# Optimization experiments

Measured on AMD Instinct MI355X. Metric: run time of the kernel, lower is better.

The kernel has to match this reference:

```python
import jax, jax.numpy as jnp
import numpy as np

N_DRUG, N_CELL, N_GENE = 2048, 2048, 4096
N = N_DRUG + N_CELL + N_GENE
E = 262144
H1, H2, H3, HEADS = 256, 64, 64, 4
N_PAIRS = 10000
EPS = 1e-5


def _gatv2(x, src, dst, Wl, bl, Wr, br, att, bias, heads, out_ch):
    # PyG GATv2Conv: e_ij = att . leaky_relu(Wl x_j + Wr x_i), softmax over incoming edges of i,
    # out_i = sum_j alpha_ij * (Wl x_j), heads concatenated, plus output bias.
    n = x.shape[0]
    xl = (x @ Wl + bl).reshape(n, heads, out_ch)   # source transform
    xr = (x @ Wr + br).reshape(n, heads, out_ch)   # target transform
    e = jax.nn.leaky_relu(xl[src] + xr[dst], 0.2)  # [E, H, C]
    logits = jnp.einsum('ehc,hc->eh', e, att)      # [E, H]
    m = jax.ops.segment_max(logits, dst, num_segments=n)
    ex = jnp.exp(logits - m[dst])
    denom = jax.ops.segment_sum(ex, dst, num_segments=n)
    alpha = ex / denom[dst]                        # [E, H]
    out = jax.ops.segment_sum(xl[src] * alpha[:, :, None], dst, num_segments=n)
    return out.reshape(n, heads * out_ch) + bias, alpha


def _graph_norm(x, gamma, beta, mscale):
    # PyG GraphNorm over a single graph: out = (x - a*mean) / sqrt(var + eps) * gamma + beta
    mu = x.mean(0)
    sub = x - mu * mscale
    var = (sub * sub).mean(0)
    return sub / jnp.sqrt(var + EPS) * gamma + beta


def setup_inputs() -> dict:
    key = jax.random.key(0)
    ks = jax.random.split(key, 24)
    f = jnp.float32
    nrm = lambda k, shape, sc: jax.random.normal(k, shape, f) * sc
    drug = jax.random.normal(ks[0], (N_DRUG, N_DRUG), f)
    cell = jax.random.normal(ks[1], (N_CELL, N_CELL), f)
    gene = jax.random.normal(ks[2], (N_GENE, N_GENE), f)
    # random edges guaranteed to have no self loops (PyG would remove then re-add them)
    src = jax.random.randint(ks[3], (E,), 0, N)
    off = jax.random.randint(ks[4], (E,), 1, N)
    edges = jnp.stack([src, (src + off) % N]).astype(jnp.int32)
    idx_drug = jax.random.randint(ks[5], (N_PAIRS,), 0, N_DRUG)
    idx_cell = N_DRUG + jax.random.randint(ks[6], (N_PAIRS,), 0, N_CELL)
    HC2, HC3 = HEADS * H2, HEADS * H3
    return {
        'drug': drug, 'cell': cell, 'gene': gene,
        'edges': edges, 'idx_drug': idx_drug, 'idx_cell': idx_cell,
        'W_drug': nrm(ks[7], (N_DRUG, H1), 1 / np.sqrt(N_DRUG)), 'b_drug': jnp.zeros((H1,), f),
        'W_cell': nrm(ks[8], (N_CELL, H1), 1 / np.sqrt(N_CELL)), 'b_cell': jnp.zeros((H1,), f),
        'W_gene': nrm(ks[9], (N_GENE, H1), 1 / np.sqrt(N_GENE)), 'b_gene': jnp.zeros((H1,), f),
        'gat1_Wl': nrm(ks[10], (H1, HC2), 1 / np.sqrt(H1)), 'gat1_bl': jnp.zeros((HC2,), f),
        'gat1_Wr': nrm(ks[11], (H1, HC2), 1 / np.sqrt(H1)), 'gat1_br': jnp.zeros((HC2,), f),
        'gat1_att': nrm(ks[12], (HEADS, H2), 1 / np.sqrt(H2)), 'gat1_bias': jnp.zeros((HC2,), f),
        'gat2_Wl': nrm(ks[13], (HC2, HC3), 1 / np.sqrt(HC2)), 'gat2_bl': jnp.zeros((HC3,), f),
        'gat2_Wr': nrm(ks[14], (HC2, HC3), 1 / np.sqrt(HC2)), 'gat2_br': jnp.zeros((HC3,), f),
        'gat2_att': nrm(ks[15], (HEADS, H3), 1 / np.sqrt(H3)), 'gat2_bias': jnp.zeros((HC3,), f),
        'gn1_gamma': jnp.ones((HC2,), f), 'gn1_beta': jnp.zeros((HC2,), f), 'gn1_scale': jnp.ones((HC2,), f),
        'gn2_gamma': jnp.ones((HC3,), f), 'gn2_beta': jnp.zeros((HC3,), f), 'gn2_scale': jnp.ones((HC3,), f),
        'lin1_W': nrm(ks[16], (2 * HC3, 1), 1 / np.sqrt(2 * HC3)), 'lin1_b': jnp.zeros((1,), f),
    }


def reference(drug, cell, gene, edges, idx_drug, idx_cell,
              W_drug, b_drug, W_cell, b_cell, W_gene, b_gene,
              gat1_Wl, gat1_bl, gat1_Wr, gat1_br, gat1_att, gat1_bias,
              gat2_Wl, gat2_bl, gat2_Wr, gat2_br, gat2_att, gat2_bias,
              gn1_gamma, gn1_beta, gn1_scale, gn2_gamma, gn2_beta, gn2_scale,
              lin1_W, lin1_b):
    x = jnp.concatenate([drug @ W_drug + b_drug,
                         cell @ W_cell + b_cell,
                         gene @ W_gene + b_gene], axis=0)  # [N, H1]
    loops = jnp.arange(N, dtype=edges.dtype)
    src = jnp.concatenate([edges[0], loops])  # GATv2Conv adds self loops
    dst = jnp.concatenate([edges[1], loops])
    x, a1 = _gatv2(x, src, dst, gat1_Wl, gat1_bl, gat1_Wr, gat1_br, gat1_att, gat1_bias, HEADS, H2)
    x = jax.nn.relu(_graph_norm(x, gn1_gamma, gn1_beta, gn1_scale))  # dropout = identity (eval)
    x, a2 = _gatv2(x, src, dst, gat2_Wl, gat2_bl, gat2_Wr, gat2_br, gat2_att, gat2_bias, HEADS, H3)
    x = jax.nn.relu(_graph_norm(x, gn2_gamma, gn2_beta, gn2_scale))
    pair = jnp.concatenate([x[idx_drug], x[idx_cell]], axis=1)  # [P, 2*H*H3]
    pred = jax.nn.sigmoid(pair @ lin1_W + lin1_b)
    # get_attention_mat: dense [N,N], every edge position set to the (detached) scalar mean of
    # attention weights; the two layer matrices share edge positions so they simply add.
    val = jax.lax.stop_gradient(a1.mean() + a2.mean())
    attn = jnp.zeros((N, N), x.dtype).at[src, dst].set(val)
    return pred, attn
```

## Files before the change

### kernel.cpp

```cpp
#include <hip/hip_runtime.h>

#define NNODES 8192
#define NEDGE  262144
#define EETOT  270336
#define NPAIRS 10000

typedef __attribute__((ext_vector_type(8))) short s16x8;
typedef __attribute__((ext_vector_type(8))) unsigned short u16x8;
typedef __attribute__((ext_vector_type(4))) float f32x4;

__device__ __forceinline__ float lrelu(float v) { return v > 0.f ? v : 0.2f * v; }

__device__ __forceinline__ void split2(float a, unsigned short& h, unsigned short& l) {
  unsigned u = __float_as_uint(a);
  h = (unsigned short)(u >> 16);
  float hf = __uint_as_float(u & 0xffff0000u);
  float r = a - hf;
  unsigned v = __float_as_uint(r);
  v += 0x7fffu + ((v >> 16) & 1u);
  l = (unsigned short)(v >> 16);
}

__device__ __forceinline__ unsigned short f2bf(float f) {
  unsigned u = __float_as_uint(f);
  u += 0x7fffu + ((u >> 16) & 1u);
  return (unsigned short)(u >> 16);
}
__device__ __forceinline__ float bf2f(unsigned short u) {
  return __uint_as_float((unsigned)u << 16);
}

__device__ __forceinline__ void wsplit_body(const float* __restrict__ W,
    unsigned short* __restrict__ Th, int K, int blk) {
  int col = threadIdx.x;
  int kb = blk * 8;
  u16x8 vh;
#pragma unroll
  for (int i = 0; i < 8; ++i)
    vh[i] = f2bf(W[(size_t)(kb + i) * 256 + col]);
  *(u16x8*)(Th + (size_t)col * K + kb) = vh;
}

__global__ __launch_bounds__(256) void k_wsplit_all(
    const float* __restrict__ Wd, const float* __restrict__ Wc, const float* __restrict__ Wg,
    const float* __restrict__ W1l, const float* __restrict__ W1r,
    const float* __restrict__ W2l, const float* __restrict__ W2r,
    unsigned short* __restrict__ tdh, unsigned short* __restrict__ tch,
    unsigned short* __restrict__ tgh,
    unsigned short* __restrict__ tl1h, unsigned short* __restrict__ tr1h,
    unsigned short* __restrict__ tl2h, unsigned short* __restrict__ tr2h,
    int* __restrict__ counts_d, int* __restrict__ counts_s, float* __restrict__ stats) {
  int b = blockIdx.x;
  if      (b < 256)  wsplit_body(Wd,  tdh, 2048, b);
  else if (b < 512)  wsplit_body(Wc,  tch, 2048, b - 256);
  else if (b < 1024) wsplit_body(Wg,  tgh, 4096, b - 512);
  else if (b < 1056) { wsplit_body(W1l, tl1h, 256, b - 1024);
                       counts_d[(b - 1024) * 256 + threadIdx.x] = 0; }
  else if (b < 1088) { wsplit_body(W1r, tr1h, 256, b - 1056);
                       counts_s[(b - 1056) * 256 + threadIdx.x] = 0; }
  else if (b < 1120) { wsplit_body(W2l, tl2h, 256, b - 1088);
                       if (b < 1092) stats[(b - 1088) * 256 + threadIdx.x] = 0.f; }
  else               wsplit_body(W2r, tr2h, 256, b - 1120);
}

struct Tile128 {
  unsigned short Ah[128][40], Al[128][40], Bh[128][40];
};
struct TileN {
  Tile128 t;
  float nsc[256], nsh[256];
};

template<bool BIAS, bool OUTBF, bool NORM>
__device__ __forceinline__ void gemm_tile128(Tile128& s,
    const float* __restrict__ A, int lda,
    const unsigned short* __restrict__ Th, int ldb, int nsteps,
    const float* __restrict__ bias, float* __restrict__ C,
    unsigned short* __restrict__ Cb,
    const float* __restrict__ nsc, const float* __restrict__ nsh) {
  const int tid = threadIdx.x;
  const int wave = tid >> 6, lane = tid & 63;
  const int g = lane >> 4, r = lane & 15;
  const int wr = (wave >> 1) * 64, wc = (wave & 1) * 64;

  const int ar = tid >> 1, ak = (tid & 1) * 16;
  const float* Arow = A + (size_t)ar * lda + ak;
  const int bc = tid & 127, bk = (tid >> 7) * 16;
  const unsigned short* Bhs = Th + (size_t)bc * ldb + bk;

  f32x4 acc[4][4];
#pragma unroll
  for (int m = 0; m < 4; ++m)
#pragma unroll
    for (int n = 0; n < 4; ++n)
#pragma unroll
      for (int j = 0; j < 4; ++j) acc[m][n][j] = 0.f;

  float4 pa0 = *(const float4*)(Arow);
  float4 pa1 = *(const float4*)(Arow + 4);
  float4 pa2 = *(const float4*)(Arow + 8);
  float4 pa3 = *(const float4*)(Arow + 12);
  u16x8 ph0 = *(const u16x8*)(Bhs);
  u16x8 ph1 = *(const u16x8*)(Bhs + 8);

  for (int t = 0; t < nsteps; ++t) {
    {
      float av[16] = {pa0.x, pa0.y, pa0.z, pa0.w, pa1.x, pa1.y, pa1.z, pa1.w,
                      pa2.x, pa2.y, pa2.z, pa2.w, pa3.x, pa3.y, pa3.z, pa3.w};
      u16x8 vh0, vh1, vl0, vl1;
#pragma unroll
      for (int i = 0; i < 16; ++i) {
        float v = av[i];
        if constexpr (NORM) {
          int ch = t * 32 + ak + i;
          v = fmaxf(v * nsc[ch] + nsh[ch], 0.f);
        }
        unsigned short hh, ll;
        split2(v, hh, ll);
        if (i < 8) { vh0[i] = hh; vl0[i] = ll; }
        else       { vh1[i - 8] = hh; vl1[i - 8] = ll; }
      }
      *(u16x8*)&s.Ah[ar][ak]     = vh0;
      *(u16x8*)&s.Ah[ar][ak + 8] = vh1;
      *(u16x8*)&s.Al[ar][ak]     = vl0;
      *(u16x8*)&s.Al[ar][ak + 8] = vl1;
      *(u16x8*)&s.Bh[bc][bk]     = ph0;
      *(u16x8*)&s.Bh[bc][bk + 8] = ph1;
    }
    __syncthreads();
    if (t + 1 < nsteps) {
      const float* An = Arow + (size_t)(t + 1) * 32;
      pa0 = *(const float4*)(An);
      pa1 = *(const float4*)(An + 4);
      pa2 = *(const float4*)(An + 8);
      pa3 = *(const float4*)(An + 12);
      const unsigned short* Bhn = Bhs + (size_t)(t + 1) * 32;
      ph0 = *(const u16x8*)(Bhn);
      ph1 = *(const u16x8*)(Bhn + 8);
    }
    s16x8 fah[4], fal[4], fbh[4];
#pragma unroll
    for (int m = 0; m < 4; ++m) {
      fah[m] = *(const s16x8*)&s.Ah[wr + m * 16 + r][g * 8];
      fal[m] = *(const s16x8*)&s.Al[wr + m * 16 + r][g * 8];
    }
#pragma unroll
    for (int n = 0; n < 4; ++n)
      fbh[n] = *(const s16x8*)&s.Bh[wc + n * 16 + r][g * 8];
#pragma unroll
    for (int m = 0; m < 4; ++m)
#pragma unroll
      for (int n = 0; n < 4; ++n) {
        acc[m][n] = __builtin_amdgcn_mfma_f32_16x16x32_bf16(fal[m], fbh[n], acc[m][n], 0, 0, 0);
        acc[m][n] = __builtin_amdgcn_mfma_f32_16x16x32_bf16(fah[m], fbh[n], acc[m][n], 0, 0, 0);
      }
    __syncthreads();
  }
#pragma unroll
  for (int m = 0; m < 4; ++m)
#pragma unroll
    for (int n = 0; n < 4; ++n) {
      int col = wc + n * 16 + r;
      float bv = BIAS ? bias[col] : 0.f;
      int rowb = wr + m * 16 + g * 4;
#pragma unroll
      for (int j = 0; j < 4; ++j) {
        float v = acc[m][n][j] + bv;
        if constexpr (OUTBF) Cb[(size_t)(rowb + j) * 256 + col] = f2bf(v);
        else                 C[(size_t)(rowb + j) * 256 + col] = v;
      }
    }
}

#define PDRUG_PLANE ((size_t)2048 * 256)
#define PGENE_PLANE ((size_t)4096 * 256)
__global__ __launch_bounds__(256) void k_inproj_fill(
    const float* __restrict__ drug, const float* __restrict__ cell,
    const float* __restrict__ gene,
    const unsigned short* __restrict__ tdh, const unsigned short* __restrict__ tch,
    const unsigned short* __restrict__ tgh, float* __restrict__ P,
    const int* __restrict__ csrdst, const int* __restrict__ rowst_s,
    float* __restrict__ attn) {
  __shared__ Tile128 s;
  int b = blockIdx.x;
  if (b >= 768) {
    int row = b - 768;
    float* rp = attn + (size_t)row * NNODES;
    f32x4* p4 = (f32x4*)rp;
    f32x4 z = {0.f, 0.f, 0.f, 0.f};
#pragma unroll
    for (int j = 0; j < 8; ++j)
      __builtin_nontemporal_store(z, p4 + j * 256 + threadIdx.x);
    __syncthreads();
    int e0 = rowst_s[row], e1 = rowst_s[row + 1];
    for (int j = e0 + (int)threadIdx.x; j < e1; j += 256)
      rp[csrdst[j]] = 16384.0f / 270336.0f;
    return;
  }
  if (b < 256) {
    int idx = b & 127;
    int colblk = (idx >> 3) & 1;
    int rest = (idx & 7) | ((idx >> 4) << 3);
    int rowblk = rest >> 2, chunk = rest & 3;
    const float* X = (b < 128) ? drug : cell;
    const unsigned short* Th = (b < 128) ? tdh : tch;
    float* Pb = P + ((b < 128) ? 0 : 4 * PDRUG_PLANE);
    gemm_tile128<false, false, false>(s,
        X + (size_t)rowblk * 128 * 2048 + (size_t)chunk * 512, 2048,
        Th + (size_t)colblk * 128 * 2048 + chunk * 512, 2048, 16, nullptr,
        Pb + (size_t)chunk * PDRUG_PLANE + (size_t)rowblk * 128 * 256 + colblk * 128,
        nullptr, nullptr, nullptr);
  } else {
    int idx = b - 256;
    int colblk = (idx >> 3) & 1;
    int rest = (idx & 7) | ((idx >> 4) << 3);
    int rowblk = rest >> 3, chunk = rest & 7;
    gemm_tile128<false, false, false>(s,
        gene + (size_t)rowblk * 128 * 4096 + (size_t)chunk * 512, 4096,
        tgh + (size_t)colblk * 128 * 4096 + chunk * 512, 4096, 16, nullptr,
        P + 8 * PDRUG_PLANE + (size_t)chunk * PGENE_PLANE + (size_t)rowblk * 128 * 256 + colblk * 128,
        nullptr, nullptr, nullptr);
  }
}

__global__ __launch_bounds__(256) void k_reduce(const float* __restrict__ P,
    const float* __restrict__ bd, const float* __restrict__ bc,
    const float* __restrict__ bg, float* __restrict__ out) {
  int idx = blockIdx.x * 256 + threadIdx.x;
  size_t e = (size_t)idx * 4;
  int row = (int)(e >> 8);
  int col = (int)(e & 255);
  const float* base; const float* bias; size_t plane; int np;
  if (row < 2048) {
    base = P + (size_t)row * 256 + col; bias = bd; plane = PDRUG_PLANE; np = 4;
  } else if (row < 4096) {
    base = P + 4 * PDRUG_PLANE + (size_t)(row - 2048) * 256 + col; bias = bc;
    plane = PDRUG_PLANE; np = 4;
  } else {
    base = P + 8 * PDRUG_PLANE + (size_t)(row - 4096) * 256 + col; bias = bg;
    plane = PGENE_PLANE; np = 8;
  }
  float4 s = *(const float4*)(base);
  for (int p = 1; p < np; ++p) {
    float4 v = *(const float4*)(base + p * plane);
    s.x += v.x; s.y += v.y; s.z += v.z; s.w += v.w;
  }
  float4 bv = *(const float4*)(bias + col);
  s.x += bv.x; s.y += bv.y; s.z += bv.z; s.w += bv.w;
  *(float4*)(out + e) = s;
}

template<bool NORM>
__global__ __launch_bounds__(256) void k_gemm2(const float* __restrict__ A,
    const unsigned short* __restrict__ ThL, const unsigned short* __restrict__ ThR,
    const float* __restrict__ biasL, const float* __restrict__ biasR,
    unsigned short* __restrict__ CLb, float* __restrict__ CR,
    const float* __restrict__ csum, const float* __restrict__ csumsq,
    const float* __restrict__ gamma, const float* __restrict__ beta,
    const float* __restrict__ mscale) {
  __shared__ TileN s;
  int b = blockIdx.x;
  int sub = (b >> 3) & 3;
  int x = (b & 7) | ((b >> 5) << 3);
  if constexpr (NORM) {
    int c = threadIdx.x;
    float mu = csum[c] * (1.0f / 8192.0f);
    float ex2 = csumsq[c] * (1.0f / 8192.0f);
    float smu = mscale[c] * mu;
    float var = ex2 - 2.f * smu * mu + smu * smu;
    float sc = rsqrtf(var + 1e-5f) * gamma[c];
    s.nsc[c] = sc;
    s.nsh[c] = beta[c] - smu * sc;
    __syncthreads();
  }
  int row0 = x * 128;
  int col0 = (sub & 1) * 128;
  if (sub >= 2) {
    gemm_tile128<true, false, NORM>(s.t, A + (size_t)row0 * 256, 256,
        ThR + (size_t)col0 * 256, 256, 8,
        biasR + col0, CR + (size_t)row0 * 256 + col0, nullptr, s.nsc, s.nsh);
  } else {
    gemm_tile128<true, true, NORM>(s.t, A + (size_t)row0 * 256, 256,
        ThL + (size_t)col0 * 256, 256, 8,
        biasL + col0, nullptr, CLb + (size_t)row0 * 256 + col0, s.nsc, s.nsh);
  }
}

__global__ void k_count2(const int* __restrict__ edges, int* __restrict__ cd,
                         int* __restrict__ cs) {
  int e = blockIdx.x * blockDim.x + threadIdx.x;
  if (e >= EETOT) return;
  int s, d;
  if (e < NEDGE) { s = edges[e]; d = edges[NEDGE + e]; } else { s = d = e - NEDGE; }
  atomicAdd(&cd[d], 1);
  atomicAdd(&cs[s], 1);
}

__global__ __launch_bounds__(1024) void k_scan2(
    const int* __restrict__ c0, int* __restrict__ r0, int* __restrict__ u0,
    const int* __restrict__ c1, int* __restrict__ r1, int* __restrict__ u1) {
  const int* counts = blockIdx.x ? c1 : c0;
  int* row_start = blockIdx.x ? r1 : r0;
  int* cursor = blockIdx.x ? u1 : u0;
  __shared__ int part[1024];
  int t = threadIdx.x;
  int base = t * 8;
  int loc[8];
  int s = 0;
#pragma unroll
  for (int j = 0; j < 8; ++j) { loc[j] = s; s += counts[base + j]; }
  part[t] = s;
  __syncthreads();
  for (int off = 1; off < 1024; off <<= 1) {
    int v = (t >= off) ? part[t - off] : 0;
    __syncthreads();
    part[t] += v;
    __syncthreads();
  }
  int pre = (t == 0) ? 0 : part[t - 1];
#pragma unroll
  for (int j = 0; j < 8; ++j) {
    int v = pre + loc[j];
    row_start[base + j] = v;
    cursor[base + j] = v;
  }
  if (t == 1023) row_start[NNODES] = pre + s;
}

__global__ void k_place2(const int* __restrict__ edges, int* __restrict__ curd,
    int* __restrict__ curs, int* __restrict__ csrsrc, int* __restrict__ csrdst) {
  int e = blockIdx.x * blockDim.x + threadIdx.x;
  if (e >= EETOT) return;
  int s, d;
  if (e < NEDGE) { s = edges[e]; d = edges[NEDGE + e]; } else { s = d = e - NEDGE; }
  int pd = atomicAdd(&curd[d], 1);
  csrsrc[pd] = s;
  int ps = atomicAdd(&curs[s], 1);
  csrdst[ps] = d;
}

__global__ __launch_bounds__(256) void k_gat(
    const unsigned short* __restrict__ xl, const float* __restrict__ xr,
    const float* __restrict__ att, const int* __restrict__ csrsrc,
    const int* __restrict__ row_start, const float* __restrict__ bias,
    float* __restrict__ out) {
  int i = blockIdx.x * 4 + (threadIdx.x >> 6);
  int lane = threadIdx.x & 63;
  int co = (lane >> 4) * 64 + (lane & 15) * 4;
  float4 w4 = *(const float4*)(att + co);
  float4 r4 = *(const float4*)(xr + (size_t)i * 256 + co);
  float sum = 0.f, ax = 0.f, ay = 0.f, az = 0.f, aw = 0.f;
  int e0 = row_start[i], e1 = row_start[i + 1];

  auto g = [&](int p) {
    int s = csrsrc[p];
    return *(const ushort4*)(xl + (size_t)s * 256 + co);
  };
  ushort4 c0, c1, c2, c3, n0, n1, n2, n3;
  int curn = min(e1 - e0, 4);
  int base = e0;
  if (curn > 0) c0 = g(base);
  if (curn > 1) c1 = g(base + 1);
  if (curn > 2) c2 = g(base + 2);
  if (curn > 3) c3 = g(base + 3);
  base += curn;
  for (;;) {
    int nxtn = min(e1 - base, 4);
    if (nxtn > 0) n0 = g(base);
    if (nxtn > 1) n1 = g(base + 1);
    if (nxtn > 2) n2 = g(base + 2);
    if (nxtn > 3) n3 = g(base + 3);
#pragma unroll
    for (int j = 0; j < 4; ++j) {
      if (j >= curn) break;
      ushort4 u = (j == 0) ? c0 : (j == 1) ? c1 : (j == 2) ? c2 : c3;
      float x0 = bf2f(u.x), x1 = bf2f(u.y), x2 = bf2f(u.z), x3 = bf2f(u.w);
      float t = w4.x * lrelu(x0 + r4.x) + w4.y * lrelu(x1 + r4.y) +
                w4.z * lrelu(x2 + r4.z) + w4.w * lrelu(x3 + r4.w);
      t += __shfl_xor(t, 1);
      t += __shfl_xor(t, 2);
      t += __shfl_xor(t, 4);
      t += __shfl_xor(t, 8);
      float el = __expf(fminf(t, 60.f));
      sum += el;
      ax += el * x0; ay += el * x1; az += el * x2; aw += el * x3;
    }
    if (nxtn <= 0) break;
    c0 = n0; c1 = n1; c2 = n2; c3 = n3;
    curn = nxtn; base += nxtn;
  }
  float inv = 1.0f / sum;
  float4 bv = *(const float4*)(bias + co);
  float4 r;
  r.x = ax * inv + bv.x; r.y = ay * inv + bv.y;
  r.z = az * inv + bv.z; r.w = aw * inv + bv.w;
  *(float4*)(out + (size_t)i * 256 + co) = r;
}

__global__ __launch_bounds__(256) void k_colstats(const float* __restrict__ x,
    float* __restrict__ csum, float* __restrict__ csumsq) {
  int c = threadIdx.x;
  int r0 = blockIdx.x * 32;
  float s = 0.f, s2 = 0.f;
  for (int r = 0; r < 32; ++r) {
    float v = x[(size_t)(r0 + r) * 256 + c];
    s += v; s2 += v * v;
  }
  atomicAdd(&csum[c], s);
  atomicAdd(&csumsq[c], s2);
}

__global__ __launch_bounds__(256) void k_pred(const float* __restrict__ h,
    const int* __restrict__ idx_drug, const int* __restrict__ idx_cell,
    const float* __restrict__ W, const float* __restrict__ b,
    const float* __restrict__ csum, const float* __restrict__ csumsq,
    const float* __restrict__ gamma, const float* __restrict__ beta,
    const float* __restrict__ mscale, float* __restrict__ out) {
  int p = blockIdx.x * 4 + (threadIdx.x >> 6);
  if (p >= NPAIRS) return;
  int lane = threadIdx.x & 63;
  int rd = idx_drug[p], rc = idx_cell[p];
  float4 a  = *(const float4*)(h + (size_t)rd * 256 + lane * 4);
  float4 cg = *(const float4*)(h + (size_t)rc * 256 + lane * 4);
  float4 wa = *(const float4*)(W + lane * 4);
  float4 wc = *(const float4*)(W + 256 + lane * 4);
  float av[4] = {a.x, a.y, a.z, a.w};
  float cv[4] = {cg.x, cg.y, cg.z, cg.w};
  float wv[4] = {wa.x, wa.y, wa.z, wa.w};
  float uv[4] = {wc.x, wc.y, wc.z, wc.w};
  float t = 0.f;
#pragma unroll
  for (int j = 0; j < 4; ++j) {
    int ch = lane * 4 + j;
    float mu = csum[ch] * (1.0f / 8192.0f);
    float ex2 = csumsq[ch] * (1.0f / 8192.0f);
    float smu = mscale[ch] * mu;
    float var = ex2 - 2.f * smu * mu + smu * smu;
    float sc = rsqrtf(var + 1e-5f) * gamma[ch];
    float sh = beta[ch] - smu * sc;
    t += fmaxf(av[j] * sc + sh, 0.f) * wv[j] + fmaxf(cv[j] * sc + sh, 0.f) * uv[j];
  }
#pragma unroll
  for (int off = 1; off < 64; off <<= 1) t += __shfl_xor(t, off);
  if (lane == 0) out[p] = 1.0f / (1.0f + __expf(-(t + b[0])));
}

extern "C" void kernel_launch(void* const* d_in, const int* in_sizes, int n_in,
                              void* d_out, int out_size, void* d_ws, size_t ws_size,
                              hipStream_t stream) {
  const float* drug = (const float*)d_in[0];
  const float* cell = (const float*)d_in[1];
  const float* gene = (const float*)d_in[2];
  const int*   edges = (const int*)d_in[3];
  const int*   idxd = (const int*)d_in[4];
  const int*   idxc = (const int*)d_in[5];
  const float* Wd = (const float*)d_in[6];   const float* bd = (const float*)d_in[7];
  const float* Wc = (const float*)d_in[8];   const float* bc = (const float*)d_in[9];
  const float* Wg = (const float*)d_in[10];  const float* bg = (const float*)d_in[11];
  const float* g1Wl = (const float*)d_in[12]; const float* g1bl = (const float*)d_in[13];
  const float* g1Wr = (const float*)d_in[14]; const float* g1br = (const float*)d_in[15];
  const float* g1att = (const float*)d_in[16]; const float* g1bias = (const float*)d_in[17];
  const float* g2Wl = (const float*)d_in[18]; const float* g2bl = (const float*)d_in[19];
  const float* g2Wr = (const float*)d_in[20]; const float* g2br = (const float*)d_in[21];
  const float* g2att = (const float*)d_in[22]; const float* g2bias = (const float*)d_in[23];
  const float* gn1g = (const float*)d_in[24]; const float* gn1b = (const float*)d_in[25];
  const float* gn1s = (const float*)d_in[26];
  const float* gn2g = (const float*)d_in[27]; const float* gn2b = (const float*)d_in[28];
  const float* gn2s = (const float*)d_in[29];
  const float* linW = (const float*)d_in[30]; const float* linb = (const float*)d_in[31];
  float* out = (float*)d_out;
  (void)in_sizes; (void)n_in; (void)out_size; (void)ws_size;

  char* ws = (char*)d_ws;
  size_t off = 0;
  auto take = [&](size_t bytes) -> void* {
    void* p = ws + off;
    off += (bytes + 255) & ~(size_t)255;
    return p;
  };
  float* bufA = (float*)take((size_t)NNODES * 256 * 4);
  unsigned short* bufBb = (unsigned short*)take((size_t)NNODES * 256 * 2);
  float* bufC = (float*)take((size_t)NNODES * 256 * 4);
  int* counts_d = (int*)take((size_t)NNODES * 4);
  int* counts_s = (int*)take((size_t)NNODES * 4);
  float* stats  = (float*)take(4 * 256 * 4);
  int* rowst_d  = (int*)take((size_t)(NNODES + 1) * 4);
  int* rowst_s  = (int*)take((size_t)(NNODES + 1) * 4);
  int* cursor_d = (int*)take((size_t)NNODES * 4);
  int* cursor_s = (int*)take((size_t)NNODES * 4);
  int* csrsrc   = (int*)take((size_t)EETOT * 4);
  int* csrdst   = (int*)take((size_t)EETOT * 4);
  unsigned short* tdh = (unsigned short*)take((size_t)256 * 2048 * 2);
  unsigned short* tch = (unsigned short*)take((size_t)256 * 2048 * 2);
  unsigned short* tgh = (unsigned short*)take((size_t)256 * 4096 * 2);
  unsigned short* tl1h = (unsigned short*)take((size_t)256 * 256 * 2);
  unsigned short* tr1h = (unsigned short*)take((size_t)256 * 256 * 2);
  unsigned short* tl2h = (unsigned short*)take((size_t)256 * 256 * 2);
  unsigned short* tr2h = (unsigned short*)take((size_t)256 * 256 * 2);
  float* Ppart = (float*)take((8 * PDRUG_PLANE + 8 * PGENE_PLANE) * 4);

  k_wsplit_all<<<1152, 256, 0, stream>>>(Wd, Wc, Wg, g1Wl, g1Wr, g2Wl, g2Wr,
      tdh, tch, tgh, tl1h, tr1h, tl2h, tr2h, counts_d, counts_s, stats);

  k_count2<<<EETOT / 256, 256, 0, stream>>>(edges, counts_d, counts_s);
  k_scan2<<<2, 1024, 0, stream>>>(counts_d, rowst_d, cursor_d, counts_s, rowst_s, cursor_s);
  k_place2<<<EETOT / 256, 256, 0, stream>>>(edges, cursor_d, cursor_s, csrsrc, csrdst);

  k_inproj_fill<<<768 + NNODES, 256, 0, stream>>>(drug, cell, gene, tdh, tch, tgh,
      Ppart, csrdst, rowst_s, out + NPAIRS);
  k_reduce<<<NNODES * 256 / 4 / 256, 256, 0, stream>>>(Ppart, bd, bc, bg, bufA);

  k_gemm2<false><<<256, 256, 0, stream>>>(bufA, tl1h, tr1h, g1bl, g1br,
      bufBb, bufC, nullptr, nullptr, nullptr, nullptr, nullptr);
  k_gat<<<NNODES / 4, 256, 0, stream>>>(bufBb, bufC, g1att, csrsrc, rowst_d, g1bias, bufA);
  k_colstats<<<NNODES / 32, 256, 0, stream>>>(bufA, stats, stats + 256);

  k_gemm2<true><<<256, 256, 0, stream>>>(bufA, tl2h, tr2h, g2bl, g2br,
      bufBb, bufC, stats, stats + 256, gn1g, gn1b, gn1s);
  k_gat<<<NNODES / 4, 256, 0, stream>>>(bufBb, bufC, g2att, csrsrc, rowst_d, g2bias, bufA);
  k_colstats<<<NNODES / 32, 256, 0, stream>>>(bufA, stats + 512, stats + 768);

  k_pred<<<NPAIRS / 4, 256, 0, stream>>>(bufA, idxd, idxc, linW, linb,
      stats + 512, stats + 768, gn2g, gn2b, gn2s, out);
}
```

Before: 299.2 us.

## Drop split-K in input projection GEMMs and fuse bias into epilogue

The input projection GEMMs no longer split K into 4–8 partial planes followed by a separate reduction kernel. Each 128x128 tile now covers the full K range and adds the bias directly in its epilogue, writing straight into bufA. This removes a large partial-sum buffer write/read and one kernel launch. In exchange only 128 GEMM blocks run instead of 768, and each loops over far more K iterations, so parallelism drops and the tail may grow unless the attention-fill blocks cover the gap.

```diff
diff --git a/kernel.cpp b/kernel.cpp
--- a/kernel.cpp
+++ b/kernel.cpp
@@ -172,19 +172,19 @@
     }
 }
 
-#define PDRUG_PLANE ((size_t)2048 * 256)
-#define PGENE_PLANE ((size_t)4096 * 256)
 __global__ __launch_bounds__(256) void k_inproj_fill(
     const float* __restrict__ drug, const float* __restrict__ cell,
     const float* __restrict__ gene,
     const unsigned short* __restrict__ tdh, const unsigned short* __restrict__ tch,
-    const unsigned short* __restrict__ tgh, float* __restrict__ P,
+    const unsigned short* __restrict__ tgh,
+    const float* __restrict__ bd, const float* __restrict__ bc,
+    const float* __restrict__ bg, float* __restrict__ bufA,
     const int* __restrict__ csrdst, const int* __restrict__ rowst_s,
     float* __restrict__ attn) {
   __shared__ Tile128 s;
   int b = blockIdx.x;
-  if (b >= 768) {
-    int row = b - 768;
+  if (b >= 128) {
+    int row = b - 128;
     float* rp = attn + (size_t)row * NNODES;
     f32x4* p4 = (f32x4*)rp;
     f32x4 z = {0.f, 0.f, 0.f, 0.f};
@@ -197,57 +197,30 @@
       rp[csrdst[j]] = 16384.0f / 270336.0f;
     return;
   }
-  if (b < 256) {
-    int idx = b & 127;
-    int colblk = (idx >> 3) & 1;
-    int rest = (idx & 7) | ((idx >> 4) << 3);
-    int rowblk = rest >> 2, chunk = rest & 3;
-    const float* X = (b < 128) ? drug : cell;
-    const unsigned short* Th = (b < 128) ? tdh : tch;
-    float* Pb = P + ((b < 128) ? 0 : 4 * PDRUG_PLANE);
-    gemm_tile128<false, false, false>(s,
-        X + (size_t)rowblk * 128 * 2048 + (size_t)chunk * 512, 2048,
-        Th + (size_t)colblk * 128 * 2048 + chunk * 512, 2048, 16, nullptr,
-        Pb + (size_t)chunk * PDRUG_PLANE + (size_t)rowblk * 128 * 256 + colblk * 128,
+  int grp = b >> 5;
+  int idx = b & 31;
+  int colblk = (idx >> 3) & 1;
+  int rest = (idx & 7) | ((idx >> 4) << 3);
+  if (grp < 2) {
+    int rowblk = rest;
+    const float* X = grp ? cell : drug;
+    const unsigned short* Th = grp ? tch : tdh;
+    const float* bias = grp ? bc : bd;
+    float* C = bufA + (size_t)grp * 2048 * 256;
+    gemm_tile128<true, false, false>(s,
+        X + (size_t)rowblk * 128 * 2048, 2048,
+        Th + (size_t)colblk * 128 * 2048, 2048, 64, bias + colblk * 128,
+        C + (size_t)rowblk * 128 * 256 + colblk * 128, nullptr, nullptr, nullptr);
+  } else {
+    int gi = b - 64;
+    int colblk2 = (gi >> 3) & 1;
+    int rowblk = (gi & 7) | ((gi >> 4) << 3);
+    gemm_tile128<true, false, false>(s,
+        gene + (size_t)rowblk * 128 * 4096, 4096,
+        tgh + (size_t)colblk2 * 128 * 4096, 4096, 128, bg + colblk2 * 128,
+        bufA + (size_t)4096 * 256 + (size_t)rowblk * 128 * 256 + colblk2 * 128,
         nullptr, nullptr, nullptr);
-  } else {
-    int idx = b - 256;
-    int colblk = (idx >> 3) & 1;
-    int rest = (idx & 7) | ((idx >> 4) << 3);
-    int rowblk = rest >> 3, chunk = rest & 7;
-    gemm_tile128<false, false, false>(s,
-        gene + (size_t)rowblk * 128 * 4096 + (size_t)chunk * 512, 4096,
-        tgh + (size_t)colblk * 128 * 4096 + chunk * 512, 4096, 16, nullptr,
-        P + 8 * PDRUG_PLANE + (size_t)chunk * PGENE_PLANE + (size_t)rowblk * 128 * 256 + colblk * 128,
-        nullptr, nullptr, nullptr);
-  }
-}
-
-__global__ __launch_bounds__(256) void k_reduce(const float* __restrict__ P,
-    const float* __restrict__ bd, const float* __restrict__ bc,
-    const float* __restrict__ bg, float* __restrict__ out) {
-  int idx = blockIdx.x * 256 + threadIdx.x;
-  size_t e = (size_t)idx * 4;
-  int row = (int)(e >> 8);
-  int col = (int)(e & 255);
-  const float* base; const float* bias; size_t plane; int np;
-  if (row < 2048) {
-    base = P + (size_t)row * 256 + col; bias = bd; plane = PDRUG_PLANE; np = 4;
-  } else if (row < 4096) {
-    base = P + 4 * PDRUG_PLANE + (size_t)(row - 2048) * 256 + col; bias = bc;
-    plane = PDRUG_PLANE; np = 4;
-  } else {
-    base = P + 8 * PDRUG_PLANE + (size_t)(row - 4096) * 256 + col; bias = bg;
-    plane = PGENE_PLANE; np = 8;
-  }
-  float4 s = *(const float4*)(base);
-  for (int p = 1; p < np; ++p) {
-    float4 v = *(const float4*)(base + p * plane);
-    s.x += v.x; s.y += v.y; s.z += v.z; s.w += v.w;
-  }
-  float4 bv = *(const float4*)(bias + col);
-  s.x += bv.x; s.y += bv.y; s.z += bv.z; s.w += bv.w;
-  *(float4*)(out + e) = s;
+  }
 }
 
 template<bool NORM>
@@ -497,7 +470,6 @@
   unsigned short* tr1h = (unsigned short*)take((size_t)256 * 256 * 2);
   unsigned short* tl2h = (unsigned short*)take((size_t)256 * 256 * 2);
   unsigned short* tr2h = (unsigned short*)take((size_t)256 * 256 * 2);
-  float* Ppart = (float*)take((8 * PDRUG_PLANE + 8 * PGENE_PLANE) * 4);
 
   k_wsplit_all<<<1152, 256, 0, stream>>>(Wd, Wc, Wg, g1Wl, g1Wr, g2Wl, g2Wr,
       tdh, tch, tgh, tl1h, tr1h, tl2h, tr2h, counts_d, counts_s, stats);
@@ -506,9 +478,8 @@
   k_scan2<<<2, 1024, 0, stream>>>(counts_d, rowst_d, cursor_d, counts_s, rowst_s, cursor_s);
   k_place2<<<EETOT / 256, 256, 0, stream>>>(edges, cursor_d, cursor_s, csrsrc, csrdst);
 
-  k_inproj_fill<<<768 + NNODES, 256, 0, stream>>>(drug, cell, gene, tdh, tch, tgh,
-      Ppart, csrdst, rowst_s, out + NPAIRS);
-  k_reduce<<<NNODES * 256 / 4 / 256, 256, 0, stream>>>(Ppart, bd, bc, bg, bufA);
+  k_inproj_fill<<<128 + NNODES, 256, 0, stream>>>(drug, cell, gene, tdh, tch, tgh,
+      bd, bc, bg, bufA, csrdst, rowst_s, out + NPAIRS);
 
   k_gemm2<false><<<256, 256, 0, stream>>>(bufA, tl1h, tr1h, g1bl, g1br,
       bufBb, bufC, nullptr, nullptr, nullptr, nullptr, nullptr);
```

Measured after the change: 378.6 us. 1.27x slower.
